# Kernel tuning notes

Hardware: AMD Instinct MI355X
Metric: run time of the kernel (lower is better)

## Reference

```python
import jax, jax.numpy as jnp
import numpy as np

B, T, M, D = 2, 2048, 2048, 128
H = M // D
ROTARY_BASE = 10000
NORM_EPS = 1e-6
QK_SCALE = 1.0 / D  # mult = sqrt(qk_scale) applied to both q and k
INFTY_APPROX = 1e30


def setup_inputs() -> dict:
    key = jax.random.key(0)
    ks = jax.random.split(key, 6)
    w_scale = M ** (-0.5)
    return {
        "x": jax.random.normal(ks[0], (B, T, M), jnp.float32),
        "wq": jax.random.normal(ks[1], (M, H, D), jnp.float32) * w_scale,
        "wk": jax.random.normal(ks[2], (M, H, D), jnp.float32) * w_scale,
        "wv": jax.random.normal(ks[3], (M, H, D), jnp.float32) * w_scale,
        "wo": jax.random.normal(ks[4], (H, D, M), jnp.float32) * w_scale,
        "gq": jnp.zeros((H, 1, D), jnp.float32),
        "bq": jnp.zeros((H, 1, D), jnp.float32),
        "gk": jnp.zeros((H, 1, D), jnp.float32),
        "bk": jnp.zeros((H, 1, D), jnp.float32),
    }


def _qk_layernorm(x, g, b):
    # x: [B,H,T,D]; g,b: [H,1,D]; centered RMS norm with trainable (1+g), b
    x = x - jnp.mean(x, axis=-1, keepdims=True)
    x = x / jnp.sqrt(jnp.mean(jnp.square(x), axis=-1, keepdims=True) + NORM_EPS)
    return x * (1.0 + g)[None] + b[None]


def _rotary(x):
    # x: [B,H,T,D]; half-split rotary encoding
    half = D // 2
    positions = jnp.arange(T, dtype=jnp.float32)[:, None]          # [T,1]
    ang_freqs = jnp.power(float(ROTARY_BASE), -jnp.arange(half, dtype=jnp.float32) / half)[None, :]  # [1,half]
    radians = positions * ang_freqs                                  # [T,half]
    cos = jnp.cos(radians)[None, None].astype(x.dtype)               # [1,1,T,half]
    sin = jnp.sin(radians)[None, None].astype(x.dtype)
    even, odd = jnp.split(x, 2, axis=-1)
    return jnp.concatenate([even * cos - odd * sin, even * sin + odd * cos], axis=-1)


def reference(x, wq, wk, wv, wo, gq, bq, gk, bk):
    q = jnp.einsum('bim,mhd->bhid', x, wq)
    k = jnp.einsum('bim,mhd->bhid', x, wk)
    v = jnp.einsum('bim,mhd->bhid', x, wv)
    q = _rotary(_qk_layernorm(q, gq, bq))
    k = _rotary(_qk_layernorm(k, gk, bk))
    mult = jnp.asarray(QK_SCALE ** 0.5, dtype=x.dtype)
    s = jnp.einsum('bhid,bhjd->bhij', q * mult, k * mult)            # [B,H,T,T]
    i = jnp.arange(T)[:, None]
    j = jnp.arange(T)[None, :]
    future = (i < j)[None, None]                                      # mask future positions
    s = s - jnp.asarray(INFTY_APPROX, dtype=s.dtype) * future
    p = jax.nn.softmax(s, axis=-1)
    o = jnp.einsum('bhij,bhjd->bhid', p, v)
    return jnp.einsum('bhid,hdm->bim', o, wo)
```

## Files before the change

kernel.cpp:

```cpp
#include <hip/hip_runtime.h>


#define NB 2
#define NT 2048
#define NM 2048
#define NH 16
#define ND 128

typedef __attribute__((ext_vector_type(4))) float f32x4;
typedef __attribute__((ext_vector_type(8))) short bf16x8;
typedef __attribute__((ext_vector_type(4))) short bf16x4;

#define AS1 __attribute__((address_space(1)))
#define AS3 __attribute__((address_space(3)))

__device__ __forceinline__ unsigned short f2bf(float f){
  unsigned int u = __float_as_uint(f);
  u = (u + 0x7fffu + ((u >> 16) & 1u)) >> 16;
  return (unsigned short)u;
}
__device__ __forceinline__ float bf2f(short s){
  return __uint_as_float(((unsigned int)(unsigned short)s) << 16);
}
__device__ __forceinline__ float wredsum(float v){
  #pragma unroll
  for (int m = 1; m < 64; m <<= 1) v += __shfl_xor(v, m);
  return v;
}
__device__ __forceinline__ void gload_lds16(const void* g, void* l){
  __builtin_amdgcn_global_load_lds((const AS1 void*)g, (AS3 void*)l, 16, 0, 0);
}

__global__ __launch_bounds__(64) void rope_table_k(float* ctab, float* stab){
  int t = blockIdx.x, i = threadIdx.x;
  float freq = __expf(-(float)i * (9.210340371976184f / 64.0f));
  float ang = (float)t * freq;
  ctab[t * 64 + i] = cosf(ang);
  stab[t * 64 + i] = sinf(ang);
}

__global__ __launch_bounds__(256) void cast_x_k(const float* __restrict__ x,
                                                short* __restrict__ xb){
  size_t gid = (size_t)blockIdx.x * 256 + threadIdx.x;
  float4 v = *(const float4*)(x + gid * 4);
  bf16x4 o;
  o[0] = (short)f2bf(v.x); o[1] = (short)f2bf(v.y);
  o[2] = (short)f2bf(v.z); o[3] = (short)f2bf(v.w);
  *(bf16x4*)(xb + gid * 4) = o;
}

__global__ __launch_bounds__(256) void transpose_w_k(const float* __restrict__ wq,
                                                     const float* __restrict__ wk,
                                                     const float* __restrict__ wv,
                                                     const float* __restrict__ wo,
                                                     short* __restrict__ wT){
  __shared__ float tl[32][33];
  int z = blockIdx.z;
  const float* src = (z == 0) ? wq : (z == 1) ? wk : (z == 2) ? wv : wo;
  short* dst = wT + (size_t)z * 2048 * 2048;
  int n0 = blockIdx.x * 32, k0 = blockIdx.y * 32;
  int cx = threadIdx.x & 31, ry = threadIdx.x >> 5;
  #pragma unroll
  for (int p = 0; p < 4; ++p)
    tl[ry + 8 * p][cx] = src[(size_t)(k0 + ry + 8 * p) * 2048 + n0 + cx];
  __syncthreads();
  #pragma unroll
  for (int p = 0; p < 4; ++p)
    dst[(size_t)(n0 + ry + 8 * p) * 2048 + k0 + cx] =
        (short)f2bf(tl[cx][ry + 8 * p]);
}

#define NKT 32
__global__ __launch_bounds__(512, 2) void gemm256_k(const short* __restrict__ A,
                                                    const short* __restrict__ Bt,
                                                    short* __restrict__ Cq){
  extern __shared__ char lds[];
  const int tid = threadIdx.x;
  const int wid = tid >> 6, lane = tid & 63;
  const int lrow = lane & 15, g8 = lane >> 4;
  const int wm = wid >> 2, wn = wid & 3;
  const int Kdim = 2048;

  int bid = blockIdx.x;
  int s = (bid & 7) * 48 + (bid >> 3);
  const int bx = s & 15;
  const int by = s >> 4;
  const int m0 = bx * 256, n0 = by * 256;

  const int r8 = lane >> 3;
  const int gcol = ((lane & 7) ^ r8) * 8;
  const short* Ab = A  + (size_t)(m0 + wid * 8 + r8) * Kdim + gcol;
  const short* Bb = Bt + (size_t)(n0 + wid * 8 + r8) * Kdim + gcol;

  f32x4 acc[8][4] = {};

  auto STAGE = [&](int c, int kt){
    #pragma unroll
    for (int h = 0; h < 2; ++h)
      #pragma unroll
      for (int l = 0; l < 2; ++l){
        size_t roff = (size_t)(h * 128 + l * 64) * Kdim + kt * 64;
        char* la = lds + c * 32768 + h * 16384 + l * 8192 + wid * 1024;
        gload_lds16(Ab + roff, la);
        gload_lds16(Bb + roff, la + 65536);
      }
  };
  auto ldA = [&](int c, int mi, int kk) -> bf16x8 {
    int row = mi * 16 + lrow;
    int col = (kk * 64 + g8 * 16) ^ ((lrow & 7) << 4);
    return *(const bf16x8*)(lds + c * 32768 + wm * 16384 + row * 128 + col);
  };
  auto ldB = [&](int c, int ni, int kk) -> bf16x8 {
    int row = (wn & 1) * 64 + ni * 16 + lrow;
    int col = (kk * 64 + g8 * 16) ^ ((lrow & 7) << 4);
    return *(const bf16x8*)(lds + 65536 + c * 32768 + (wn >> 1) * 16384 + row * 128 + col);
  };

  STAGE(0, 0);

  for (int kt = 0; kt < NKT; ++kt){
    const int c = kt & 1;
    asm volatile("s_waitcnt vmcnt(0)" ::: "memory");
    __builtin_amdgcn_s_barrier();
    if (kt + 1 < NKT) STAGE(c ^ 1, kt + 1);

    #pragma unroll
    for (int kk = 0; kk < 2; ++kk){
      bf16x8 bfr[4];
      #pragma unroll
      for (int ni = 0; ni < 4; ++ni) bfr[ni] = ldB(c, ni, kk);
      #pragma unroll
      for (int mh = 0; mh < 2; ++mh){
        bf16x8 afr[4];
        #pragma unroll
        for (int mi = 0; mi < 4; ++mi) afr[mi] = ldA(c, mh * 4 + mi, kk);
        #pragma unroll
        for (int mi = 0; mi < 4; ++mi)
          #pragma unroll
          for (int ni = 0; ni < 4; ++ni)
            acc[mh * 4 + mi][ni] = __builtin_amdgcn_mfma_f32_16x16x32_bf16(
                afr[mi], bfr[ni], acc[mh * 4 + mi][ni], 0, 0, 0);
      }
    }
  }

  const int tsel = by >> 3;
  short* dst = Cq + (size_t)tsel * (NB * NH * NT * ND);
  if (tsel < 2){
    #pragma unroll
    for (int mi = 0; mi < 8; ++mi){
      int rowb = m0 + wm * 128 + mi * 16 + g8 * 4;
      #pragma unroll
      for (int ni = 0; ni < 4; ++ni){
        int col = n0 + wn * 64 + ni * 16 + lrow;
        int hd = col & 2047;
        int hh = hd >> 7, d = hd & 127;
        f32x4 a = acc[mi][ni];
        #pragma unroll
        for (int r = 0; r < 4; ++r){
          int bt = rowb + r;
          int b = bt >> 11, t = bt & 2047;
          dst[(((size_t)(b * NH + hh)) * NT + t) * ND + d] = (short)f2bf(a[r]);
        }
      }
    }
  } else {
    #pragma unroll
    for (int mi = 0; mi < 8; ++mi){
      int rowb = m0 + wm * 128 + mi * 16 + g8 * 4;
      int b = rowb >> 11, t0 = rowb & 2047;
      int jb = t0 >> 6, toff = t0 & 63;
      #pragma unroll
      for (int ni = 0; ni < 4; ++ni){
        int col = n0 + wn * 64 + ni * 16 + lrow;
        int hd = col & 2047;
        int hh = hd >> 7, d = hd & 127;
        f32x4 a = acc[mi][ni];
        bf16x4 w4;
        #pragma unroll
        for (int r = 0; r < 4; ++r) w4[r] = (short)f2bf(a[r]);
        *(bf16x4*)&dst[(((size_t)(b * NH + hh) * 32 + jb) * ND + d) * 64 + toff] = w4;
      }
    }
  }
}

__global__ __launch_bounds__(256) void gemm_bt_k(const short* __restrict__ A,
                                                 const short* __restrict__ Bt,
                                                 float* __restrict__ Cout,
                                                 int Kdim){
  __shared__ short As[2][128 * 32];
  __shared__ short Bs[2][128 * 32];
  const int tid = threadIdx.x;
  const int wid = tid >> 6, lane = tid & 63;
  const int lrow = lane & 15, g8 = lane >> 4;
  const int wm = wid >> 1, wn = wid & 1;
  const int m0 = blockIdx.x * 128, n0 = blockIdx.y * 128;
  f32x4 acc[4][4] = {};
  const int srow = lane >> 2;
  const int skcol = (lane & 3) * 8;

  auto STAGE = [&](int c, int kt){
    #pragma unroll
    for (int i = 0; i < 2; ++i){
      int inst = wid * 2 + i;
      int r = inst * 16 + srow;
      const short* sa = A  + (size_t)(m0 + r) * Kdim + kt + skcol;
      const short* sb = Bt + (size_t)(n0 + r) * Kdim + kt + skcol;
      gload_lds16(sa, (char*)As[c] + inst * 1024);
      gload_lds16(sb, (char*)Bs[c] + inst * 1024);
    }
  };

  STAGE(0, 0);
  const int nkt = Kdim >> 5;
  for (int it = 0; it < nkt; ++it){
    const int c = it & 1;
    asm volatile("s_waitcnt vmcnt(0)" ::: "memory");
    __builtin_amdgcn_s_barrier();
    if (it + 1 < nkt) STAGE(c ^ 1, (it + 1) << 5);

    bf16x8 af[4], bfv[4];
    #pragma unroll
    for (int mi = 0; mi < 4; ++mi)
      af[mi] = *(const bf16x8*)&As[c][(wm * 64 + mi * 16 + lrow) * 32 + g8 * 8];
    #pragma unroll
    for (int ni = 0; ni < 4; ++ni)
      bfv[ni] = *(const bf16x8*)&Bs[c][(wn * 64 + ni * 16 + lrow) * 32 + g8 * 8];
    #pragma unroll
    for (int mi = 0; mi < 4; ++mi)
      #pragma unroll
      for (int ni = 0; ni < 4; ++ni)
        acc[mi][ni] = __builtin_amdgcn_mfma_f32_16x16x32_bf16(
            af[mi], bfv[ni], acc[mi][ni], 0, 0, 0);
  }

  #pragma unroll
  for (int mi = 0; mi < 4; ++mi){
    int rowb = m0 + wm * 64 + mi * 16 + g8 * 4;
    #pragma unroll
    for (int ni = 0; ni < 4; ++ni){
      int col = n0 + wn * 64 + ni * 16 + lrow;
      f32x4 a = acc[mi][ni];
      #pragma unroll
      for (int r = 0; r < 4; ++r)
        Cout[(size_t)(rowb + r) * 2048 + col] = a[r];
    }
  }
}

__global__ __launch_bounds__(256) void norm_rope_k(const short* __restrict__ qkv,
                                                   short* __restrict__ outp,
                                                   const float* __restrict__ gq,
                                                   const float* __restrict__ bq,
                                                   const float* __restrict__ gk,
                                                   const float* __restrict__ bk,
                                                   const float* __restrict__ ctab,
                                                   const float* __restrict__ stab){
  int which = blockIdx.y;
  const short* src = qkv + (size_t)which * (NB * NH * NT * ND);
  short* dst = outp + (size_t)which * (NB * NH * NT * ND);
  const float* g = which ? gk : gq;
  const float* bb = which ? bk : bq;
  const float qs = which ? 1.0f : 0.011271055007f;
  int wid = threadIdx.x >> 6, lane = threadIdx.x & 63;
  size_t row = (size_t)blockIdx.x * 4 + wid;
  int h = (int)((row >> 11) & 15);
  int t = (int)(row & 2047);
  const short* rp = src + row * ND;
  float v0 = bf2f(rp[lane]), v1 = bf2f(rp[lane + 64]);
  float mean = wredsum(v0 + v1) * (1.0f / 128.0f);
  float c0 = v0 - mean, c1 = v1 - mean;
  float ms = wredsum(c0 * c0 + c1 * c1) * (1.0f / 128.0f);
  float rstd = rsqrtf(ms + 1e-6f);
  float n0 = c0 * rstd * (1.0f + g[h * ND + lane]) + bb[h * ND + lane];
  float n1 = c1 * rstd * (1.0f + g[h * ND + lane + 64]) + bb[h * ND + lane + 64];
  float co = ctab[t * 64 + lane], si = stab[t * 64 + lane];
  short* wp = dst + row * ND;
  wp[lane]      = (short)f2bf((n0 * co - n1 * si) * qs);
  wp[lane + 64] = (short)f2bf((n0 * si + n1 * co) * qs);
}

__global__ __launch_bounds__(256) void attn_k(const short* __restrict__ qn,
                                              const short* __restrict__ kn,
                                              const short* __restrict__ vt,
                                              short* __restrict__ ob){
  extern __shared__ char lds[];
  const int tid = threadIdx.x;
  const int wid = tid >> 6, lane = tid & 63;
  const int lrow = lane & 15, g8 = lane >> 4;
  const int id = blockIdx.x;
  const int qx = id >> 5;
  const int bh = id & 31;
  const int b = bh >> 4, h = bh & 15;
  const size_t base = (size_t)bh * NT * ND;
  char* Pw = lds + 65536 + wid * 2048;

  auto STAGE = [&](int cb, int jb){
    #pragma unroll
    for (int i = 0; i < 4; ++i){
      int r0 = wid * 16 + i * 4;
      int r = r0 + (lane >> 4);
      int g = lane & 15;
      gload_lds16(kn + base + (size_t)(jb * 64 + r) * ND + ((g ^ (r & 7)) << 3),
                  lds + cb * 16384 + r0 * 256);
    }
    #pragma unroll
    for (int i = 0; i < 4; ++i){
      int d0 = wid * 32 + i * 8;
      int d = d0 + (lane >> 3);
      int g = lane & 7;
      gload_lds16(vt + base + (size_t)jb * 8192 + d * 64 + ((g ^ (d & 7)) << 3),
                  lds + 32768 + cb * 16384 + d0 * 128);
    }
  };

  for (int pass = 0; pass < 2; ++pass){
    const int qt = pass ? (31 - qx) : qx;
    const int t0 = qt * 64;
    const int tq = t0 + wid * 16 + lrow;
    bf16x8 qf[4];
    #pragma unroll
    for (int dc = 0; dc < 4; ++dc)
      qf[dc] = *(const bf16x8*)(qn + base + (size_t)tq * ND + dc * 32 + g8 * 8);
    f32x4 O[8] = {};
    float m = -3e38f, lsum = 0.0f;

    __syncthreads();
    STAGE(0, 0);

    for (int jb = 0; jb <= qt; ++jb){
      const int cb = jb & 1;
      asm volatile("s_waitcnt vmcnt(0)" ::: "memory");
      __builtin_amdgcn_s_barrier();
      if (jb < qt) STAGE(cb ^ 1, jb + 1);
      const char* Kb = lds + cb * 16384;
      const char* Vb = lds + 32768 + cb * 16384;

      if (jb * 64 <= t0 + wid * 16 + 15){
        f32x4 st[4] = {};
        __builtin_amdgcn_s_setprio(1);
        #pragma unroll
        for (int dc = 0; dc < 4; ++dc)
          #pragma unroll
          for (int js = 0; js < 4; ++js){
            int jl = js * 16 + lrow;
            bf16x8 kf = *(const bf16x8*)(Kb + jl * 256 +
                          (((dc * 4 + g8) ^ (jl & 7)) << 4));
            st[js] = __builtin_amdgcn_mfma_f32_16x16x32_bf16(kf, qf[dc], st[js], 0, 0, 0);
          }
        __builtin_amdgcn_s_setprio(0);
        if (jb == qt){
          #pragma unroll
          for (int js = 0; js < 4; ++js)
            #pragma unroll
            for (int r = 0; r < 4; ++r){
              int j = jb * 64 + js * 16 + g8 * 4 + r;
              if (j > tq) st[js][r] = -3e38f;
            }
        }
        f32x4 m4 = st[0];
        #pragma unroll
        for (int js = 1; js < 4; ++js)
          #pragma unroll
          for (int r = 0; r < 4; ++r) m4[r] = fmaxf(m4[r], st[js][r]);
        float mx = fmaxf(fmaxf(m4[0], m4[1]), fmaxf(m4[2], m4[3]));
        mx = fmaxf(mx, __shfl_xor(mx, 16));
        mx = fmaxf(mx, __shfl_xor(mx, 32));
        if (!__all(mx <= m + 8.0f)){
          float mnew = fmaxf(m, mx);
          float fac = exp2f(m - mnew);
          m = mnew;
          lsum *= fac;
          #pragma unroll
          for (int dcb = 0; dcb < 8; ++dcb) O[dcb] *= fac;
        }
        float ps = 0.0f;
        #pragma unroll
        for (int js = 0; js < 4; ++js){
          float p0 = exp2f(st[js][0] - m);
          float p1 = exp2f(st[js][1] - m);
          float p2 = exp2f(st[js][2] - m);
          float p3 = exp2f(st[js][3] - m);
          ps += (p0 + p1) + (p2 + p3);
          unsigned int lo, hi;
          asm("v_cvt_pk_bf16_f32 %0, %1, %2" : "=v"(lo) : "v"(p0), "v"(p1));
          asm("v_cvt_pk_bf16_f32 %0, %1, %2" : "=v"(hi) : "v"(p2), "v"(p3));
          uint2 w; w.x = lo; w.y = hi;
          *(uint2*)(Pw + lrow * 128 + ((js * 32 + g8 * 8) ^ ((lrow & 7) << 4))) = w;
        }
        ps += __shfl_xor(ps, 16);
        ps += __shfl_xor(ps, 32);
        lsum += ps;
        asm volatile("s_waitcnt lgkmcnt(0)" ::: "memory");
        __builtin_amdgcn_s_setprio(1);
        #pragma unroll
        for (int j32 = 0; j32 < 2; ++j32){
          bf16x8 pf = *(const bf16x8*)(Pw + lrow * 128 +
                        ((j32 * 64 + g8 * 16) ^ ((lrow & 7) << 4)));
          #pragma unroll
          for (int dcb = 0; dcb < 8; ++dcb){
            int d = dcb * 16 + lrow;
            bf16x8 vf = *(const bf16x8*)(Vb + d * 128 +
                          (((j32 * 4 + g8) ^ (d & 7)) << 4));
            O[dcb] = __builtin_amdgcn_mfma_f32_16x16x32_bf16(vf, pf, O[dcb], 0, 0, 0);
          }
        }
        __builtin_amdgcn_s_setprio(0);
      }
    }
    float inv = 1.0f / lsum;
    #pragma unroll
    for (int dcb = 0; dcb < 8; ++dcb){
      bf16x4 w4;
      #pragma unroll
      for (int r = 0; r < 4; ++r) w4[r] = (short)f2bf(O[dcb][r] * inv);
      *(bf16x4*)(ob + ((size_t)(b * NT + tq)) * (NH * ND) + h * ND + dcb * 16 + g8 * 4) = w4;
    }
  }
}

extern "C" void kernel_launch(void* const* d_in, const int* in_sizes, int n_in,
                              void* d_out, int out_size, void* d_ws, size_t ws_size,
                              hipStream_t stream){
  const float* x  = (const float*)d_in[0];
  const float* wq = (const float*)d_in[1];
  const float* wk = (const float*)d_in[2];
  const float* wv = (const float*)d_in[3];
  const float* wo = (const float*)d_in[4];
  const float* gq = (const float*)d_in[5];
  const float* bq = (const float*)d_in[6];
  const float* gk = (const float*)d_in[7];
  const float* bk = (const float*)d_in[8];

  char* ws = (char*)d_ws;
  short* xb   = (short*)(ws);
  short* wT   = (short*)(ws + 16777216);
  short* qkvb = (short*)(ws + 50331648);
  short* qkn  = (short*)(ws + 100663296);
  short* ob   = (short*)(ws + 134217728);
  float* ctab = (float*)(ws + 150994944);
  float* stab = (float*)(ws + 151519232);

  (void)hipFuncSetAttribute((const void*)gemm256_k,
                            hipFuncAttributeMaxDynamicSharedMemorySize, 131072);
  (void)hipFuncSetAttribute((const void*)attn_k,
                            hipFuncAttributeMaxDynamicSharedMemorySize, 73728);

  rope_table_k<<<dim3(2048), dim3(64), 0, stream>>>(ctab, stab);
  cast_x_k<<<dim3(8192), dim3(256), 0, stream>>>(x, xb);
  transpose_w_k<<<dim3(64, 64, 4), dim3(256), 0, stream>>>(wq, wk, wv, wo, wT);
  gemm256_k<<<dim3(384), dim3(512), 131072, stream>>>(xb, wT, qkvb);
  norm_rope_k<<<dim3(16384, 2), dim3(256), 0, stream>>>(qkvb, qkn, gq, bq, gk, bk, ctab, stab);
  attn_k<<<dim3(512), dim3(256), 73728, stream>>>(qkn, qkn + 8388608,
                                                  qkvb + 2 * (size_t)8388608, ob);
  gemm_bt_k<<<dim3(32, 16), dim3(256), 0, stream>>>(ob, wT + 3 * (size_t)4194304,
                                                    (float*)d_out, 2048);
}
```

Measured before the change: 285.7 us.

## Fuse prep kernels; enlarge attention query tiles with triple-buffered K/V staging

Merges the rope-table, x-cast and weight-transpose kernels into one prep kernel to cut launch overhead. The attention kernel now uses 8 waves per block covering 128 query rows, so each K/V tile staged in LDS is reused by twice as many waves. K/V staging becomes a three-deep ring with partial vmcnt waits so loads run two tiles ahead. The trade is higher LDS use (114 KB), fewer blocks (256), and per-wave causal masking on diagonal tiles, which may reduce occupancy or balance.

```diff
diff --git a/kernel.cpp b/kernel.cpp
--- a/kernel.cpp
+++ b/kernel.cpp
@@ -31,43 +31,47 @@
   __builtin_amdgcn_global_load_lds((const AS1 void*)g, (AS3 void*)l, 16, 0, 0);
 }
 
-__global__ __launch_bounds__(64) void rope_table_k(float* ctab, float* stab){
-  int t = blockIdx.x, i = threadIdx.x;
-  float freq = __expf(-(float)i * (9.210340371976184f / 64.0f));
-  float ang = (float)t * freq;
-  ctab[t * 64 + i] = cosf(ang);
-  stab[t * 64 + i] = sinf(ang);
-}
-
-__global__ __launch_bounds__(256) void cast_x_k(const float* __restrict__ x,
-                                                short* __restrict__ xb){
-  size_t gid = (size_t)blockIdx.x * 256 + threadIdx.x;
-  float4 v = *(const float4*)(x + gid * 4);
-  bf16x4 o;
-  o[0] = (short)f2bf(v.x); o[1] = (short)f2bf(v.y);
-  o[2] = (short)f2bf(v.z); o[3] = (short)f2bf(v.w);
-  *(bf16x4*)(xb + gid * 4) = o;
-}
-
-__global__ __launch_bounds__(256) void transpose_w_k(const float* __restrict__ wq,
-                                                     const float* __restrict__ wk,
-                                                     const float* __restrict__ wv,
-                                                     const float* __restrict__ wo,
-                                                     short* __restrict__ wT){
+__global__ __launch_bounds__(256) void prep_k(const float* __restrict__ x,
+                                              const float* __restrict__ wq,
+                                              const float* __restrict__ wk,
+                                              const float* __restrict__ wv,
+                                              const float* __restrict__ wo,
+                                              short* __restrict__ xb,
+                                              short* __restrict__ wT,
+                                              float* __restrict__ ctab,
+                                              float* __restrict__ stab){
   __shared__ float tl[32][33];
-  int z = blockIdx.z;
-  const float* src = (z == 0) ? wq : (z == 1) ? wk : (z == 2) ? wv : wo;
-  short* dst = wT + (size_t)z * 2048 * 2048;
-  int n0 = blockIdx.x * 32, k0 = blockIdx.y * 32;
-  int cx = threadIdx.x & 31, ry = threadIdx.x >> 5;
-  #pragma unroll
-  for (int p = 0; p < 4; ++p)
-    tl[ry + 8 * p][cx] = src[(size_t)(k0 + ry + 8 * p) * 2048 + n0 + cx];
-  __syncthreads();
-  #pragma unroll
-  for (int p = 0; p < 4; ++p)
-    dst[(size_t)(n0 + ry + 8 * p) * 2048 + k0 + cx] =
-        (short)f2bf(tl[cx][ry + 8 * p]);
+  const int bid = blockIdx.x, tid = threadIdx.x;
+  if (bid < 8192){
+    size_t gid = (size_t)bid * 256 + tid;
+    float4 v = *(const float4*)(x + gid * 4);
+    bf16x4 o;
+    o[0] = (short)f2bf(v.x); o[1] = (short)f2bf(v.y);
+    o[2] = (short)f2bf(v.z); o[3] = (short)f2bf(v.w);
+    *(bf16x4*)(xb + gid * 4) = o;
+  } else if (bid < 24576){
+    int tb = bid - 8192;
+    int z = tb >> 12, rem = tb & 4095;
+    int n0 = (rem & 63) * 32, k0 = (rem >> 6) * 32;
+    const float* src = (z == 0) ? wq : (z == 1) ? wk : (z == 2) ? wv : wo;
+    short* dst = wT + (size_t)z * 2048 * 2048;
+    int cx = tid & 31, ry = tid >> 5;
+    #pragma unroll
+    for (int p = 0; p < 4; ++p)
+      tl[ry + 8 * p][cx] = src[(size_t)(k0 + ry + 8 * p) * 2048 + n0 + cx];
+    __syncthreads();
+    #pragma unroll
+    for (int p = 0; p < 4; ++p)
+      dst[(size_t)(n0 + ry + 8 * p) * 2048 + k0 + cx] =
+          (short)f2bf(tl[cx][ry + 8 * p]);
+  } else {
+    int t = (bid - 24576) * 4 + (tid >> 6);
+    int i = tid & 63;
+    float freq = __expf(-(float)i * (9.210340371976184f / 64.0f));
+    float ang = (float)t * freq;
+    ctab[t * 64 + i] = cosf(ang);
+    stab[t * 64 + i] = sinf(ang);
+  }
 }
 
 #define NKT 32
@@ -281,7 +285,7 @@
   wp[lane + 64] = (short)f2bf((n0 * si + n1 * co) * qs);
 }
 
-__global__ __launch_bounds__(256) void attn_k(const short* __restrict__ qn,
+__global__ __launch_bounds__(512) void attn_k(const short* __restrict__ qn,
                                               const short* __restrict__ kn,
                                               const short* __restrict__ vt,
                                               short* __restrict__ ob){
@@ -290,54 +294,58 @@
   const int wid = tid >> 6, lane = tid & 63;
   const int lrow = lane & 15, g8 = lane >> 4;
   const int id = blockIdx.x;
-  const int qx = id >> 5;
+  const int qs = id >> 5;
   const int bh = id & 31;
   const int b = bh >> 4, h = bh & 15;
   const size_t base = (size_t)bh * NT * ND;
-  char* Pw = lds + 65536 + wid * 2048;
-
-  auto STAGE = [&](int cb, int jb){
-    #pragma unroll
-    for (int i = 0; i < 4; ++i){
-      int r0 = wid * 16 + i * 4;
+  char* Pw = lds + 98304 + wid * 2048;
+
+  auto STAGE = [&](int jb){
+    const int cb = jb % 3;
+    #pragma unroll
+    for (int i = 0; i < 2; ++i){
+      int r0 = wid * 4 + i * 32;
       int r = r0 + (lane >> 4);
       int g = lane & 15;
       gload_lds16(kn + base + (size_t)(jb * 64 + r) * ND + ((g ^ (r & 7)) << 3),
                   lds + cb * 16384 + r0 * 256);
     }
     #pragma unroll
-    for (int i = 0; i < 4; ++i){
-      int d0 = wid * 32 + i * 8;
+    for (int i = 0; i < 2; ++i){
+      int d0 = wid * 8 + i * 64;
       int d = d0 + (lane >> 3);
       int g = lane & 7;
       gload_lds16(vt + base + (size_t)jb * 8192 + d * 64 + ((g ^ (d & 7)) << 3),
-                  lds + 32768 + cb * 16384 + d0 * 128);
+                  lds + 49152 + cb * 16384 + d0 * 128);
     }
   };
 
   for (int pass = 0; pass < 2; ++pass){
-    const int qt = pass ? (31 - qx) : qx;
-    const int t0 = qt * 64;
-    const int tq = t0 + wid * 16 + lrow;
+    const int qt = pass ? (15 - qs) : qs;
+    const int t0 = qt * 128;
+    const int wrow0 = t0 + wid * 16;
+    const int tq = wrow0 + lrow;
     bf16x8 qf[4];
     #pragma unroll
     for (int dc = 0; dc < 4; ++dc)
       qf[dc] = *(const bf16x8*)(qn + base + (size_t)tq * ND + dc * 32 + g8 * 8);
     f32x4 O[8] = {};
     float m = -3e38f, lsum = 0.0f;
+    const int ntiles = 2 * qt + 2;
 
     __syncthreads();
-    STAGE(0, 0);
-
-    for (int jb = 0; jb <= qt; ++jb){
-      const int cb = jb & 1;
-      asm volatile("s_waitcnt vmcnt(0)" ::: "memory");
+    STAGE(0);
+    STAGE(1);
+
+    for (int jb = 0; jb < ntiles; ++jb){
+      if (jb + 1 < ntiles) asm volatile("s_waitcnt vmcnt(4)" ::: "memory");
+      else                 asm volatile("s_waitcnt vmcnt(0)" ::: "memory");
       __builtin_amdgcn_s_barrier();
-      if (jb < qt) STAGE(cb ^ 1, jb + 1);
-      const char* Kb = lds + cb * 16384;
-      const char* Vb = lds + 32768 + cb * 16384;
-
-      if (jb * 64 <= t0 + wid * 16 + 15){
+      if (jb + 2 < ntiles) STAGE(jb + 2);
+      const char* Kb = lds + (jb % 3) * 16384;
+      const char* Vb = lds + 49152 + (jb % 3) * 16384;
+
+      if (jb * 64 <= wrow0 + 15){
         f32x4 st[4] = {};
         __builtin_amdgcn_s_setprio(1);
         #pragma unroll
@@ -350,7 +358,7 @@
             st[js] = __builtin_amdgcn_mfma_f32_16x16x32_bf16(kf, qf[dc], st[js], 0, 0, 0);
           }
         __builtin_amdgcn_s_setprio(0);
-        if (jb == qt){
+        if (jb * 64 + 63 > wrow0){
           #pragma unroll
           for (int js = 0; js < 4; ++js)
             #pragma unroll
@@ -445,15 +453,13 @@
   (void)hipFuncSetAttribute((const void*)gemm256_k,
                             hipFuncAttributeMaxDynamicSharedMemorySize, 131072);
   (void)hipFuncSetAttribute((const void*)attn_k,
-                            hipFuncAttributeMaxDynamicSharedMemorySize, 73728);
-
-  rope_table_k<<<dim3(2048), dim3(64), 0, stream>>>(ctab, stab);
-  cast_x_k<<<dim3(8192), dim3(256), 0, stream>>>(x, xb);
-  transpose_w_k<<<dim3(64, 64, 4), dim3(256), 0, stream>>>(wq, wk, wv, wo, wT);
+                            hipFuncAttributeMaxDynamicSharedMemorySize, 114688);
+
+  prep_k<<<dim3(25088), dim3(256), 0, stream>>>(x, wq, wk, wv, wo, xb, wT, ctab, stab);
   gemm256_k<<<dim3(384), dim3(512), 131072, stream>>>(xb, wT, qkvb);
   norm_rope_k<<<dim3(16384, 2), dim3(256), 0, stream>>>(qkvb, qkn, gq, bq, gk, bk, ctab, stab);
-  attn_k<<<dim3(512), dim3(256), 73728, stream>>>(qkn, qkn + 8388608,
-                                                  qkvb + 2 * (size_t)8388608, ob);
+  attn_k<<<dim3(256), dim3(512), 114688, stream>>>(qkn, qkn + 8388608,
+                                                   qkvb + 2 * (size_t)8388608, ob);
   gemm_bt_k<<<dim3(32, 16), dim3(256), 0, stream>>>(ob, wT + 3 * (size_t)4194304,
                                                     (float*)d_out, 2048);
 }
```

Measured after the change: 277.2 us. -3.0%, faster.
